# Kernel tuning notes

Hardware: AMD Instinct MI355X
Metric: run time of the kernel (lower is better)

The kernel has to match this reference:

```python
import jax, jax.numpy as jnp
import numpy as np

CODEBOOK_DIM = 12          # log2(codebook_size)
CODEBOOK_SIZE = 4096
DIM = 512
INV_TEMPERATURE = 100.0
CODEBOOK_SCALE = 1.0
DIVERSITY_GAMMA = 1.0
ENTROPY_LOSS_WEIGHT = 0.1
EPS = 1e-5


def setup_inputs() -> dict:
    key = jax.random.key(0)
    k_x, k_wi, k_wo = jax.random.split(key, 3)
    x = jax.random.normal(k_x, (4, 4096, DIM), dtype=jnp.float32)
    # nn.Linear weights: (out_features, in_features)
    w_in = jax.random.normal(k_wi, (CODEBOOK_DIM, DIM), dtype=jnp.float32) * 0.02
    b_in = jnp.zeros((CODEBOOK_DIM,), dtype=jnp.float32)
    w_out = jax.random.normal(k_wo, (DIM, CODEBOOK_DIM), dtype=jnp.float32) * 0.02
    b_out = jnp.zeros((DIM,), dtype=jnp.float32)
    return {"x": x, "w_in": w_in, "b_in": b_in, "w_out": w_out, "b_out": b_out}


def _entropy(prob):
    return (-prob * jnp.log(jnp.clip(prob, EPS))).sum(axis=-1)


def _make_codebook():
    mask = (2 ** jnp.arange(CODEBOOK_DIM - 1, -1, -1)).astype(jnp.int32)  # [d]
    all_codes = jnp.arange(CODEBOOK_SIZE, dtype=jnp.int32)
    bits = ((all_codes[:, None] & mask) != 0).astype(jnp.float32)  # [cs, d]
    codebook = bits * CODEBOOK_SCALE * 2 - CODEBOOK_SCALE  # {-1, +1}
    return mask, codebook


def reference(x, w_in, b_in, w_out, b_out):
    mask, codebook = _make_codebook()

    # project in: [b, n, dim] -> [b, n, d]
    xp = jnp.einsum('bnd,cd->bnc', x, w_in) + b_in  # c == codebook_dim here

    # sign quantization (num_codebooks = 1, so c-dim is implicit)
    quantized = jnp.where(xp > 0, CODEBOOK_SCALE, -CODEBOOK_SCALE).astype(xp.dtype)
    indices = ((quantized > 0).astype(jnp.int32) * mask).sum(axis=-1)  # [b, n]

    # straight-through estimator (training path)
    x_st = xp + jax.lax.stop_gradient(quantized - xp)

    # entropy aux loss over full codebook (frac_per_sample_entropy = 1.0)
    flat = xp.reshape(-1, CODEBOOK_DIM)  # original (pre-quant) input, [bn, d]
    # -distance * inv_temp = 2 * inv_temp * <x, code>
    logits = (2.0 * INV_TEMPERATURE) * (flat @ codebook.T)  # [bn, cs]
    prob = jax.nn.softmax(logits, axis=-1)
    per_sample_entropy = _entropy(prob).mean()
    avg_prob = prob.mean(axis=0)  # [cs]
    codebook_entropy = _entropy(avg_prob)
    entropy_aux_loss = per_sample_entropy - DIVERSITY_GAMMA * codebook_entropy
    aux_loss = entropy_aux_loss * ENTROPY_LOSS_WEIGHT

    # project out: [b, n, d] -> [b, n, dim]
    out = jnp.einsum('bnc,dc->bnd', x_st, w_out) + b_out
    return out, indices, aux_loss
```

## Files before the change

### kernel.cpp

```cpp
#include <hip/hip_runtime.h>
#include <hip/hip_bf16.h>


#define NS    16384
#define NOUT  (NS*512)
#define AUXO  (NOUT+NS)
#define INVT2 200.0f
#define NBLK  512
#define RBLK  64

template <int CTRL>
__device__ inline float dpp_add(float v) {
  int p = __builtin_amdgcn_update_dpp(0, __float_as_int(v), CTRL, 0xF, 0xF, true);
  return v + __int_as_float(p);
}
__device__ inline float rdlane(float v, int lane) {
  return __int_as_float(__builtin_amdgcn_readlane(__float_as_int(v), lane));
}

__global__ __launch_bounds__(512) void k_table(const float* __restrict__ w_out,
                                               const float* __restrict__ b_out,
                                               float* __restrict__ T) {
  __shared__ float s_wt[6144];
  const int t = threadIdx.x;
  #pragma unroll
  for (int k = 0; k < 12; ++k) s_wt[t + k * 512] = w_out[t * 12 + k];
  __syncthreads();

  const int c = blockIdx.x * 16 + (t >> 5);
  float sg[12];
  #pragma unroll
  for (int d = 0; d < 12; ++d) sg[d] = ((c >> (11 - d)) & 1) ? 1.f : -1.f;

  float4* Trow = (float4*)(T + (size_t)c * 512);
  #pragma unroll
  for (int k4 = 0; k4 < 4; ++k4) {
    const int m = (t & 31) + k4 * 32;
    float4 bo = ((const float4*)b_out)[m];
    float4 o = bo;
    #pragma unroll
    for (int d = 0; d < 12; ++d) {
      float4 w4 = ((const float4*)s_wt)[d * 128 + m];
      o.x += sg[d] * w4.x; o.y += sg[d] * w4.y; o.z += sg[d] * w4.z; o.w += sg[d] * w4.w;
    }
    Trow[m] = o;
  }
}

__global__ __launch_bounds__(512, 4) void k_main(
    const float* __restrict__ x,
    const float* __restrict__ w_in,  const float* __restrict__ b_in,
    const float* __restrict__ T,
    float* __restrict__ out, float* __restrict__ idx_out,
    float* __restrict__ P, float* __restrict__ Csum) {

  __shared__ float s_wi[6144];
  __shared__ float s_phi[32][64];
  __shared__ float s_psi[32][64];
  __shared__ float s_h[8];

  const int t = threadIdx.x;

  #pragma unroll
  for (int k = 0; k < 12; ++k) {
    int f  = t + k * 512;
    int kk = f & 3;
    int q  = f >> 2;
    int sub = q & 15, e4 = (q >> 4) & 7, d = q >> 7;
    int e  = sub * 32 + e4 * 4 + kk;
    s_wi[f] = w_in[d * 512 + e];
  }
  __syncthreads();

  const int wave = t >> 6, lane = t & 63;
  const int g = lane >> 4, sub = lane & 15;

  float bin[12];
  #pragma unroll
  for (int d = 0; d < 12; ++d) bin[d] = b_in[d];

  const int i0 = blockIdx.x * 32 + wave * 4 + g;

  const float4* xr0 = (const float4*)(x + (size_t)i0 * 512 + sub * 32);
  float4 xv0[8];
  #pragma unroll
  for (int e4 = 0; e4 < 8; ++e4) xv0[e4] = xr0[e4];

  float p0[12];
  #pragma unroll
  for (int d = 0; d < 12; ++d) p0[d] = 0.f;
  #pragma unroll
  for (int e4 = 0; e4 < 8; ++e4) {
    #pragma unroll
    for (int d = 0; d < 12; ++d) {
      float4 w4 = ((const float4*)s_wi)[d * 128 + e4 * 16 + sub];
      p0[d] += xv0[e4].x * w4.x + xv0[e4].y * w4.y + xv0[e4].z * w4.z + xv0[e4].w * w4.w;
    }
  }
  #pragma unroll
  for (int d = 0; d < 12; ++d) {
    #pragma unroll
    for (int m = 1; m <= 8; m <<= 1) {
      p0[d] += __shfl_xor(p0[d], m, 16);
    }
    p0[d] += bin[d];
  }

  unsigned idx0 = 0u;
  #pragma unroll
  for (int d = 0; d < 12; ++d) {
    idx0 |= (p0[d] > 0.f ? 1u : 0u) << (11 - d);
  }
  if (sub == 0) {
    idx_out[i0] = (float)idx0;
  }

  {
    const float4* Trow = (const float4*)(T + (size_t)idx0 * 512);
    float4* or0 = (float4*)(out + (size_t)i0 * 512);
    #pragma unroll
    for (int e4 = 0; e4 < 8; ++e4) {
      or0[e4 * 16 + sub] = Trow[e4 * 16 + sub];
    }
  }

  float hacc = 0.f;
  #pragma unroll
  for (int s = 0; s < 4; ++s) {
    float xq[12];
    #pragma unroll
    for (int d = 0; d < 12; ++d) xq[d] = rdlane(p0[d], 16 * s);

    float hi = 0.f, lo = 0.f, ah = 0.f, al = 0.f;
    #pragma unroll
    for (int d = 0; d < 6; ++d) {
      int bh = (lane >> (5 - d)) & 1;
      hi += bh ? xq[d]     : -xq[d];
      lo += bh ? xq[6 + d] : -xq[6 + d];
      ah += fabsf(xq[d]);
      al += fabsf(xq[6 + d]);
    }
    float lhi = INVT2 * (hi - ah);
    float llo = INVT2 * (lo - al);
    float ehi = __expf(lhi);
    float elo = __expf(llo);

    float Shi = ehi, Slo = elo;
    Shi = dpp_add<0xB1>(Shi);  Slo = dpp_add<0xB1>(Slo);
    Shi = dpp_add<0x4E>(Shi);  Slo = dpp_add<0x4E>(Slo);
    Shi = dpp_add<0x141>(Shi); Slo = dpp_add<0x141>(Slo);
    Shi = dpp_add<0x140>(Shi); Slo = dpp_add<0x140>(Slo);
    {
      float r0 = rdlane(Shi, 0), r1 = rdlane(Shi, 16), r2 = rdlane(Shi, 32), r3 = rdlane(Shi, 48);
      Shi = (r0 + r1) + (r2 + r3);
      float q0 = rdlane(Slo, 0), q1 = rdlane(Slo, 16), q2 = rdlane(Slo, 32), q3 = rdlane(Slo, 48);
      Slo = (q0 + q1) + (q2 + q3);
    }

    float phi = ehi / Shi;
    float psi = elo / Slo;
    float lnShi = __logf(Shi), lnSlo = __logf(Slo);
    hacc += phi * (lhi - lnShi) + psi * (llo - lnSlo);

    const int ws = wave * 4 + s;
    s_phi[ws][lane] = phi;
    s_psi[ws][lane] = psi;
  }

  #pragma unroll
  for (int m = 1; m <= 32; m <<= 1) hacc += __shfl_xor(hacc, m);
  if (lane == 0) s_h[wave] = hacc;
  __syncthreads();
  if (t == 0) {
    float hs = 0.f;
    for (int w2 = 0; w2 < 8; ++w2) hs += s_h[w2];
    atomicAdd(Csum, hs);
  }

  const int jb = (t >> 5) * 4;
  const int lb = (t & 31) * 2;
  float a00 = 0.f, a01 = 0.f, a10 = 0.f, a11 = 0.f;
  float a20 = 0.f, a21 = 0.f, a30 = 0.f, a31 = 0.f;
  #pragma unroll 4
  for (int s = 0; s < 32; ++s) {
    float4 ph = *(const float4*)&s_phi[s][jb];
    float2 ps = *(const float2*)&s_psi[s][lb];
    a00 += ph.x * ps.x; a01 += ph.x * ps.y;
    a10 += ph.y * ps.x; a11 += ph.y * ps.y;
    a20 += ph.z * ps.x; a21 += ph.z * ps.y;
    a30 += ph.w * ps.x; a31 += ph.w * ps.y;
  }
  float* Pr = P + (size_t)blockIdx.x * 4096;
  *(float2*)&Pr[(jb + 0) * 64 + lb] = make_float2(a00, a01);
  *(float2*)&Pr[(jb + 1) * 64 + lb] = make_float2(a10, a11);
  *(float2*)&Pr[(jb + 2) * 64 + lb] = make_float2(a20, a21);
  *(float2*)&Pr[(jb + 3) * 64 + lb] = make_float2(a30, a31);
}

__global__ __launch_bounds__(256) void k_reduce(const float* __restrict__ P,
                                                float* __restrict__ scal,
                                                float* __restrict__ aux) {
  __shared__ float red[4][64];
  const int t = threadIdx.x;
  const int c = blockIdx.x * 64 + (t & 63);
  const int rg = t >> 6;
  float s = 0.f;
  #pragma unroll 8
  for (int j = 0; j < 128; ++j) s += P[(size_t)(rg * 128 + j) * 4096 + c];
  red[rg][t & 63] = s;
  __syncthreads();
  if (t < 64) {
    float tot = (red[0][t] + red[1][t]) + (red[2][t] + red[3][t]);
    float pb = tot * (1.f / (float)NS);
    float e = pb * __logf(fmaxf(pb, 1e-5f));
    #pragma unroll
    for (int m = 1; m <= 32; m <<= 1) e += __shfl_xor(e, m);
    if (t == 0) {
      atomicAdd(&scal[1], e);
      __threadfence();
      unsigned done = atomicAdd((unsigned*)&scal[2], 1u);
      if (done == RBLK - 1) {
        float E = atomicAdd(&scal[1], 0.f);
        float C = atomicAdd(&scal[0], 0.f);
        float per_sample_entropy = -C * (1.f / (float)NS);
        float codebook_entropy   = -E;
        aux[0] = 0.1f * (per_sample_entropy - codebook_entropy);
      }
    }
  }
}

extern "C" void kernel_launch(void* const* d_in, const int* in_sizes, int n_in,
                              void* d_out, int out_size, void* d_ws, size_t ws_size,
                              hipStream_t stream) {
  const float* x     = (const float*)d_in[0];
  const float* w_in  = (const float*)d_in[1];
  const float* b_in  = (const float*)d_in[2];
  const float* w_out = (const float*)d_in[3];
  const float* b_out = (const float*)d_in[4];
  float* out = (float*)d_out;

  float* T    = (float*)d_ws;
  float* P    = T + (size_t)4096 * 512;
  float* scal = P + (size_t)NBLK * 4096;

  hipMemsetAsync(scal, 0, 3 * sizeof(float), stream);
  k_table<<<256, 512, 0, stream>>>(w_out, b_out, T);
  k_main<<<NBLK, 512, 0, stream>>>(x, w_in, b_in, T,
                                   out, out + NOUT, P, scal);
  k_reduce<<<RBLK, 256, 0, stream>>>(P, scal, out + AUXO);
}
```

Measured before the change: 118.9 us.

## Split main kernel into projection and entropy kernels, compute output directly

Drops the precomputed 4096x512 output lookup table and computes the out-projection inline from sign bits and shared-memory w_out. Splits the fused kernel into a projection kernel, which handles two rows per 16-lane group and writes the 12-dim projections to a workspace buffer, and a separate entropy kernel that reads them and builds larger 64-sample partial outer products. This removes the table build and the gather reads of table rows, and halves the number of partial-product blocks the final reduction has to sum. The cost is an extra kernel launch, a small projection round trip through global memory, and more register pressure in the projection kernel.

```diff
diff --git a/kernel.cpp b/kernel.cpp
--- a/kernel.cpp
+++ b/kernel.cpp
@@ -6,7 +6,8 @@
 #define NOUT  (NS*512)
 #define AUXO  (NOUT+NS)
 #define INVT2 200.0f
-#define NBLK  512
+#define PBLK  256
+#define EBLK  256
 #define RBLK  64
 
 template <int CTRL>
@@ -18,50 +19,18 @@
   return __int_as_float(__builtin_amdgcn_readlane(__float_as_int(v), lane));
 }
 
-__global__ __launch_bounds__(512) void k_table(const float* __restrict__ w_out,
-                                               const float* __restrict__ b_out,
-                                               float* __restrict__ T) {
-  __shared__ float s_wt[6144];
-  const int t = threadIdx.x;
-  #pragma unroll
-  for (int k = 0; k < 12; ++k) s_wt[t + k * 512] = w_out[t * 12 + k];
-  __syncthreads();
-
-  const int c = blockIdx.x * 16 + (t >> 5);
-  float sg[12];
-  #pragma unroll
-  for (int d = 0; d < 12; ++d) sg[d] = ((c >> (11 - d)) & 1) ? 1.f : -1.f;
-
-  float4* Trow = (float4*)(T + (size_t)c * 512);
-  #pragma unroll
-  for (int k4 = 0; k4 < 4; ++k4) {
-    const int m = (t & 31) + k4 * 32;
-    float4 bo = ((const float4*)b_out)[m];
-    float4 o = bo;
-    #pragma unroll
-    for (int d = 0; d < 12; ++d) {
-      float4 w4 = ((const float4*)s_wt)[d * 128 + m];
-      o.x += sg[d] * w4.x; o.y += sg[d] * w4.y; o.z += sg[d] * w4.z; o.w += sg[d] * w4.w;
-    }
-    Trow[m] = o;
-  }
-}
-
-__global__ __launch_bounds__(512, 4) void k_main(
+__global__ __launch_bounds__(512, 2) void k_proj(
     const float* __restrict__ x,
     const float* __restrict__ w_in,  const float* __restrict__ b_in,
-    const float* __restrict__ T,
+    const float* __restrict__ w_out, const float* __restrict__ b_out,
     float* __restrict__ out, float* __restrict__ idx_out,
-    float* __restrict__ P, float* __restrict__ Csum) {
+    float* __restrict__ xp_out) {
 
   __shared__ float s_wi[6144];
-  __shared__ float s_phi[32][64];
-  __shared__ float s_psi[32][64];
-  __shared__ float s_h[8];
+  __shared__ float s_wt[6144];
 
   const int t = threadIdx.x;
 
-  #pragma unroll
   for (int k = 0; k < 12; ++k) {
     int f  = t + k * 512;
     int kk = f & 3;
@@ -69,6 +38,7 @@
     int sub = q & 15, e4 = (q >> 4) & 7, d = q >> 7;
     int e  = sub * 32 + e4 * 4 + kk;
     s_wi[f] = w_in[d * 512 + e];
+    s_wt[f] = w_out[t * 12 + k];
   }
   __syncthreads();
 
@@ -79,22 +49,25 @@
   #pragma unroll
   for (int d = 0; d < 12; ++d) bin[d] = b_in[d];
 
-  const int i0 = blockIdx.x * 32 + wave * 4 + g;
+  const int i0 = blockIdx.x * 64 + wave * 8 + g;
+  const int i1 = i0 + 4;
 
   const float4* xr0 = (const float4*)(x + (size_t)i0 * 512 + sub * 32);
-  float4 xv0[8];
-  #pragma unroll
-  for (int e4 = 0; e4 < 8; ++e4) xv0[e4] = xr0[e4];
-
-  float p0[12];
-  #pragma unroll
-  for (int d = 0; d < 12; ++d) p0[d] = 0.f;
+  const float4* xr1 = (const float4*)(x + (size_t)i1 * 512 + sub * 32);
+  float4 xv0[8], xv1[8];
+  #pragma unroll
+  for (int e4 = 0; e4 < 8; ++e4) { xv0[e4] = xr0[e4]; xv1[e4] = xr1[e4]; }
+
+  float p0[12], p1[12];
+  #pragma unroll
+  for (int d = 0; d < 12; ++d) { p0[d] = 0.f; p1[d] = 0.f; }
   #pragma unroll
   for (int e4 = 0; e4 < 8; ++e4) {
     #pragma unroll
     for (int d = 0; d < 12; ++d) {
       float4 w4 = ((const float4*)s_wi)[d * 128 + e4 * 16 + sub];
       p0[d] += xv0[e4].x * w4.x + xv0[e4].y * w4.y + xv0[e4].z * w4.z + xv0[e4].w * w4.w;
+      p1[d] += xv1[e4].x * w4.x + xv1[e4].y * w4.y + xv1[e4].z * w4.z + xv1[e4].w * w4.w;
     }
   }
   #pragma unroll
@@ -102,34 +75,78 @@
     #pragma unroll
     for (int m = 1; m <= 8; m <<= 1) {
       p0[d] += __shfl_xor(p0[d], m, 16);
+      p1[d] += __shfl_xor(p1[d], m, 16);
     }
     p0[d] += bin[d];
-  }
-
-  unsigned idx0 = 0u;
+    p1[d] += bin[d];
+  }
+
+  unsigned idx0 = 0u, idx1 = 0u;
   #pragma unroll
   for (int d = 0; d < 12; ++d) {
     idx0 |= (p0[d] > 0.f ? 1u : 0u) << (11 - d);
+    idx1 |= (p1[d] > 0.f ? 1u : 0u) << (11 - d);
   }
   if (sub == 0) {
     idx_out[i0] = (float)idx0;
+    idx_out[i1] = (float)idx1;
   }
 
   {
-    const float4* Trow = (const float4*)(T + (size_t)idx0 * 512);
-    float4* or0 = (float4*)(out + (size_t)i0 * 512);
-    #pragma unroll
-    for (int e4 = 0; e4 < 8; ++e4) {
-      or0[e4 * 16 + sub] = Trow[e4 * 16 + sub];
-    }
-  }
+    float4 v0 = make_float4(p0[0], p0[1], p0[2], p0[3]);
+    float4 v1 = make_float4(p1[0], p1[1], p1[2], p1[3]);
+    if (sub == 1) { v0 = make_float4(p0[4], p0[5], p0[6], p0[7]);
+                    v1 = make_float4(p1[4], p1[5], p1[6], p1[7]); }
+    if (sub == 2) { v0 = make_float4(p0[8], p0[9], p0[10], p0[11]);
+                    v1 = make_float4(p1[8], p1[9], p1[10], p1[11]); }
+    if (sub < 3) {
+      ((float4*)(xp_out + (size_t)i0 * 12))[sub] = v0;
+      ((float4*)(xp_out + (size_t)i1 * 12))[sub] = v1;
+    }
+  }
+
+  float sg0[12], sg1[12];
+  #pragma unroll
+  for (int d = 0; d < 12; ++d) {
+    sg0[d] = p0[d] > 0.f ? 1.f : -1.f;
+    sg1[d] = p1[d] > 0.f ? 1.f : -1.f;
+  }
+  float4* or0 = (float4*)(out + (size_t)i0 * 512);
+  float4* or1 = (float4*)(out + (size_t)i1 * 512);
+  #pragma unroll
+  for (int e4 = 0; e4 < 8; ++e4) {
+    float4 bo = ((const float4*)b_out)[e4 * 16 + sub];
+    float4 o0 = bo, o1 = bo;
+    #pragma unroll
+    for (int d = 0; d < 12; ++d) {
+      float4 w4 = ((const float4*)s_wt)[d * 128 + e4 * 16 + sub];
+      o0.x += sg0[d] * w4.x; o0.y += sg0[d] * w4.y; o0.z += sg0[d] * w4.z; o0.w += sg0[d] * w4.w;
+      o1.x += sg1[d] * w4.x; o1.y += sg1[d] * w4.y; o1.z += sg1[d] * w4.z; o1.w += sg1[d] * w4.w;
+    }
+    or0[e4 * 16 + sub] = o0;
+    or1[e4 * 16 + sub] = o1;
+  }
+}
+
+__global__ __launch_bounds__(512) void k_ent(
+    const float* __restrict__ xp,
+    float* __restrict__ P, float* __restrict__ scal) {
+
+  __shared__ float s_phi[64][64];
+  __shared__ float s_psi[64][64];
+  __shared__ float s_h[8];
+
+  const int t = threadIdx.x;
+  const int wave = t >> 6, lane = t & 63;
+  const int sbase = blockIdx.x * 64 + wave * 8;
 
   float hacc = 0.f;
-  #pragma unroll
-  for (int s = 0; s < 4; ++s) {
+  #pragma unroll 1
+  for (int s = 0; s < 8; ++s) {
+    const float* xps = xp + (size_t)(sbase + s) * 12;
     float xq[12];
     #pragma unroll
-    for (int d = 0; d < 12; ++d) xq[d] = rdlane(p0[d], 16 * s);
+    for (int d = 0; d < 12; ++d) xq[d] = xps[d];
 
     float hi = 0.f, lo = 0.f, ah = 0.f, al = 0.f;
     #pragma unroll
@@ -162,9 +179,8 @@
     float lnShi = __logf(Shi), lnSlo = __logf(Slo);
     hacc += phi * (lhi - lnShi) + psi * (llo - lnSlo);
 
-    const int ws = wave * 4 + s;
-    s_phi[ws][lane] = phi;
-    s_psi[ws][lane] = psi;
+    s_phi[wave * 8 + s][lane] = phi;
+    s_psi[wave * 8 + s][lane] = psi;
   }
 
   #pragma unroll
@@ -174,7 +190,7 @@
   if (t == 0) {
     float hs = 0.f;
     for (int w2 = 0; w2 < 8; ++w2) hs += s_h[w2];
-    atomicAdd(Csum, hs);
+    atomicAdd(&scal[0], hs);
   }
 
   const int jb = (t >> 5) * 4;
@@ -182,7 +198,7 @@
   float a00 = 0.f, a01 = 0.f, a10 = 0.f, a11 = 0.f;
   float a20 = 0.f, a21 = 0.f, a30 = 0.f, a31 = 0.f;
   #pragma unroll 4
-  for (int s = 0; s < 32; ++s) {
+  for (int s = 0; s < 64; ++s) {
     float4 ph = *(const float4*)&s_phi[s][jb];
     float2 ps = *(const float2*)&s_psi[s][lb];
     a00 += ph.x * ps.x; a01 += ph.x * ps.y;
@@ -206,7 +222,7 @@
   const int rg = t >> 6;
   float s = 0.f;
   #pragma unroll 8
-  for (int j = 0; j < 128; ++j) s += P[(size_t)(rg * 128 + j) * 4096 + c];
+  for (int j = 0; j < 64; ++j) s += P[(size_t)(rg * 64 + j) * 4096 + c];
   red[rg][t & 63] = s;
   __syncthreads();
   if (t < 64) {
@@ -240,13 +256,13 @@
   const float* b_out = (const float*)d_in[4];
   float* out = (float*)d_out;
 
-  float* T    = (float*)d_ws;
-  float* P    = T + (size_t)4096 * 512;
-  float* scal = P + (size_t)NBLK * 4096;
+  float* P    = (float*)d_ws;
+  float* xp   = P + (size_t)EBLK * 4096;
+  float* scal = xp + (size_t)NS * 12;
 
   hipMemsetAsync(scal, 0, 3 * sizeof(float), stream);
-  k_table<<<256, 512, 0, stream>>>(w_out, b_out, T);
-  k_main<<<NBLK, 512, 0, stream>>>(x, w_in, b_in, T,
-                                   out, out + NOUT, P, scal);
+  k_proj<<<PBLK, 512, 0, stream>>>(x, w_in, b_in, w_out, b_out,
+                                   out, out + NOUT, xp);
+  k_ent<<<EBLK, 512, 0, stream>>>(xp, P, scal);
   k_reduce<<<RBLK, 256, 0, stream>>>(P, scal, out + AUXO);
 }
```

Measured after the change: 116.1 us. 2.4% less time.

## Restructure into fused table+projection kernel and entropy+gather kernel, drop memset

Applied to the files above, without the earlier changes.

Folds the codebook-output table build into the same launch as the input projection, using block ranges so both run concurrently, and clears the scalar accumulators in-kernel instead of with a memset. The projected 12-dim values go to a workspace buffer. A second kernel then splits blocks between the entropy/outer-product work (64 samples per block, fewer partial rows) and the gather of output rows from the table. This removes the serial dependency of the main kernel on the table build and cuts the partial-reduction size, at the cost of an extra global round-trip for the projections and indices.

```diff
diff --git a/kernel.cpp b/kernel.cpp
--- a/kernel.cpp
+++ b/kernel.cpp
@@ -6,7 +6,10 @@
 #define NOUT  (NS*512)
 #define AUXO  (NOUT+NS)
 #define INVT2 200.0f
-#define NBLK  512
+#define TBLK  64
+#define DBLK  1024
+#define EBLK  256
+#define GBLK  512
 #define RBLK  64
 
 template <int CTRL>
@@ -18,57 +21,54 @@
   return __int_as_float(__builtin_amdgcn_readlane(__float_as_int(v), lane));
 }
 
-__global__ __launch_bounds__(512) void k_table(const float* __restrict__ w_out,
-                                               const float* __restrict__ b_out,
-                                               float* __restrict__ T) {
-  __shared__ float s_wt[6144];
-  const int t = threadIdx.x;
-  #pragma unroll
-  for (int k = 0; k < 12; ++k) s_wt[t + k * 512] = w_out[t * 12 + k];
-  __syncthreads();
-
-  const int c = blockIdx.x * 16 + (t >> 5);
-  float sg[12];
-  #pragma unroll
-  for (int d = 0; d < 12; ++d) sg[d] = ((c >> (11 - d)) & 1) ? 1.f : -1.f;
-
-  float4* Trow = (float4*)(T + (size_t)c * 512);
-  #pragma unroll
-  for (int k4 = 0; k4 < 4; ++k4) {
-    const int m = (t & 31) + k4 * 32;
-    float4 bo = ((const float4*)b_out)[m];
-    float4 o = bo;
-    #pragma unroll
-    for (int d = 0; d < 12; ++d) {
-      float4 w4 = ((const float4*)s_wt)[d * 128 + m];
-      o.x += sg[d] * w4.x; o.y += sg[d] * w4.y; o.z += sg[d] * w4.z; o.w += sg[d] * w4.w;
-    }
-    Trow[m] = o;
-  }
-}
-
-__global__ __launch_bounds__(512, 4) void k_main(
+__global__ __launch_bounds__(256) void kA(
     const float* __restrict__ x,
     const float* __restrict__ w_in,  const float* __restrict__ b_in,
-    const float* __restrict__ T,
-    float* __restrict__ out, float* __restrict__ idx_out,
-    float* __restrict__ P, float* __restrict__ Csum) {
-
-  __shared__ float s_wi[6144];
-  __shared__ float s_phi[32][64];
-  __shared__ float s_psi[32][64];
-  __shared__ float s_h[8];
-
-  const int t = threadIdx.x;
-
-  #pragma unroll
-  for (int k = 0; k < 12; ++k) {
-    int f  = t + k * 512;
-    int kk = f & 3;
-    int q  = f >> 2;
-    int sub = q & 15, e4 = (q >> 4) & 7, d = q >> 7;
-    int e  = sub * 32 + e4 * 4 + kk;
-    s_wi[f] = w_in[d * 512 + e];
+    const float* __restrict__ w_out, const float* __restrict__ b_out,
+    float* __restrict__ T, float* __restrict__ idx_out,
+    float* __restrict__ xp_out, float* __restrict__ scal) {
+
+  __shared__ float s_w[6144];
+  const int bid = blockIdx.x;
+  const int t   = threadIdx.x;
+
+  if (bid < TBLK) {
+    #pragma unroll
+    for (int k = 0; k < 12; ++k) {
+      s_w[t + k * 512]         = w_out[t * 12 + k];
+      s_w[t + 256 + k * 512]   = w_out[(t + 256) * 12 + k];
+    }
+    if (bid == 0 && t == 0) { scal[0] = 0.f; scal[1] = 0.f; ((unsigned*)scal)[2] = 0u; }
+    __syncthreads();
+
+    const int c = bid * 64 + (t >> 2);
+    float sg[12];
+    #pragma unroll
+    for (int d = 0; d < 12; ++d) sg[d] = ((c >> (11 - d)) & 1) ? 1.f : -1.f;
+
+    float4* Trow = (float4*)(T + (size_t)c * 512);
+    const float4* bo4 = (const float4*)b_out;
+    const float4* wt4 = (const float4*)s_w;
+    #pragma unroll 8
+    for (int j = 0; j < 32; ++j) {
+      const int m = (t & 3) + 4 * j;
+      float4 o = bo4[m];
+      #pragma unroll
+      for (int d = 0; d < 12; ++d) {
+        float4 w4 = wt4[d * 128 + m];
+        o.x += sg[d] * w4.x; o.y += sg[d] * w4.y; o.z += sg[d] * w4.z; o.w += sg[d] * w4.w;
+      }
+      Trow[m] = o;
+    }
+    return;
+  }
+
+  #pragma unroll
+  for (int k = 0; k < 24; ++k) {
+    const int f = t + k * 256;
+    const int d = f >> 9, e = f & 511;
+    const int pos = ((d * 128 + ((e >> 2) & 7) * 16 + (e >> 5)) << 2) | (e & 3);
+    s_w[pos] = w_in[f];
   }
   __syncthreads();
 
@@ -79,7 +79,7 @@
   #pragma unroll
   for (int d = 0; d < 12; ++d) bin[d] = b_in[d];
 
-  const int i0 = blockIdx.x * 32 + wave * 4 + g;
+  const int i0 = (bid - TBLK) * 16 + wave * 4 + g;
 
   const float4* xr0 = (const float4*)(x + (size_t)i0 * 512 + sub * 32);
   float4 xv0[8];
@@ -93,43 +93,64 @@
   for (int e4 = 0; e4 < 8; ++e4) {
     #pragma unroll
     for (int d = 0; d < 12; ++d) {
-      float4 w4 = ((const float4*)s_wi)[d * 128 + e4 * 16 + sub];
+      float4 w4 = ((const float4*)s_w)[d * 128 + e4 * 16 + sub];
       p0[d] += xv0[e4].x * w4.x + xv0[e4].y * w4.y + xv0[e4].z * w4.z + xv0[e4].w * w4.w;
     }
   }
   #pragma unroll
   for (int d = 0; d < 12; ++d) {
     #pragma unroll
-    for (int m = 1; m <= 8; m <<= 1) {
-      p0[d] += __shfl_xor(p0[d], m, 16);
-    }
+    for (int m = 1; m <= 8; m <<= 1) p0[d] += __shfl_xor(p0[d], m, 16);
     p0[d] += bin[d];
   }
 
   unsigned idx0 = 0u;
   #pragma unroll
-  for (int d = 0; d < 12; ++d) {
-    idx0 |= (p0[d] > 0.f ? 1u : 0u) << (11 - d);
-  }
-  if (sub == 0) {
-    idx_out[i0] = (float)idx0;
-  }
+  for (int d = 0; d < 12; ++d) idx0 |= (p0[d] > 0.f ? 1u : 0u) << (11 - d);
+  if (sub == 0) idx_out[i0] = (float)idx0;
 
   {
-    const float4* Trow = (const float4*)(T + (size_t)idx0 * 512);
-    float4* or0 = (float4*)(out + (size_t)i0 * 512);
-    #pragma unroll
-    for (int e4 = 0; e4 < 8; ++e4) {
-      or0[e4 * 16 + sub] = Trow[e4 * 16 + sub];
-    }
-  }
-
+    float4 v0 = make_float4(p0[0], p0[1], p0[2], p0[3]);
+    if (sub == 1) v0 = make_float4(p0[4], p0[5], p0[6], p0[7]);
+    if (sub == 2) v0 = make_float4(p0[8], p0[9], p0[10], p0[11]);
+    if (sub < 3) ((float4*)(xp_out + (size_t)i0 * 12))[sub] = v0;
+  }
+}
+
+__global__ __launch_bounds__(256) void kB(
+    const float* __restrict__ T, const float* __restrict__ idx_f,
+    const float* __restrict__ xp,
+    float* __restrict__ out, float* __restrict__ P, float* __restrict__ scal) {
+
+  __shared__ float s_phi[64][64];
+  __shared__ float s_psi[64][64];
+  __shared__ float s_h[4];
+
+  const int bid = blockIdx.x, t = threadIdx.x;
+  const int wave = t >> 6, lane = t & 63;
+
+  if (bid >= EBLK) {
+    const int base = (bid - EBLK) * 32 + wave * 8;
+    #pragma unroll
+    for (int r = 0; r < 8; ++r) {
+      const int i = base + r;
+      const unsigned c = (unsigned)idx_f[i];
+      const float4* Tr = (const float4*)(T + (size_t)c * 512);
+      float4* orow = (float4*)(out + (size_t)i * 512);
+      orow[lane]      = Tr[lane];
+      orow[lane + 64] = Tr[lane + 64];
+    }
+    return;
+  }
+
+  const int sbase = bid * 64 + wave * 16;
   float hacc = 0.f;
-  #pragma unroll
-  for (int s = 0; s < 4; ++s) {
+  #pragma unroll 1
+  for (int s = 0; s < 16; ++s) {
+    const float* xps = xp + (size_t)(sbase + s) * 12;
     float xq[12];
     #pragma unroll
-    for (int d = 0; d < 12; ++d) xq[d] = rdlane(p0[d], 16 * s);
+    for (int d = 0; d < 12; ++d) xq[d] = xps[d];
 
     float hi = 0.f, lo = 0.f, ah = 0.f, al = 0.f;
     #pragma unroll
@@ -162,51 +183,45 @@
     float lnShi = __logf(Shi), lnSlo = __logf(Slo);
     hacc += phi * (lhi - lnShi) + psi * (llo - lnSlo);
 
-    const int ws = wave * 4 + s;
-    s_phi[ws][lane] = phi;
-    s_psi[ws][lane] = psi;
+    s_phi[wave * 16 + s][lane] = phi;
+    s_psi[wave * 16 + s][lane] = psi;
   }
 
   #pragma unroll
   for (int m = 1; m <= 32; m <<= 1) hacc += __shfl_xor(hacc, m);
   if (lane == 0) s_h[wave] = hacc;
   __syncthreads();
-  if (t == 0) {
-    float hs = 0.f;
-    for (int w2 = 0; w2 < 8; ++w2) hs += s_h[w2];
-    atomicAdd(Csum, hs);
-  }
-
-  const int jb = (t >> 5) * 4;
-  const int lb = (t & 31) * 2;
-  float a00 = 0.f, a01 = 0.f, a10 = 0.f, a11 = 0.f;
-  float a20 = 0.f, a21 = 0.f, a30 = 0.f, a31 = 0.f;
+  if (t == 0) atomicAdd(&scal[0], (s_h[0] + s_h[1]) + (s_h[2] + s_h[3]));
+
+  const int jb = (t >> 4) * 4;
+  const int lb = (t & 15) * 4;
+  float4 r0 = {0,0,0,0}, r1 = {0,0,0,0}, r2 = {0,0,0,0}, r3 = {0,0,0,0};
   #pragma unroll 4
-  for (int s = 0; s < 32; ++s) {
+  for (int s = 0; s < 64; ++s) {
     float4 ph = *(const float4*)&s_phi[s][jb];
-    float2 ps = *(const float2*)&s_psi[s][lb];
-    a00 += ph.x * ps.x; a01 += ph.x * ps.y;
-    a10 += ph.y * ps.x; a11 += ph.y * ps.y;
-    a20 += ph.z * ps.x; a21 += ph.z * ps.y;
-    a30 += ph.w * ps.x; a31 += ph.w * ps.y;
-  }
-  float* Pr = P + (size_t)blockIdx.x * 4096;
-  *(float2*)&Pr[(jb + 0) * 64 + lb] = make_float2(a00, a01);
-  *(float2*)&Pr[(jb + 1) * 64 + lb] = make_float2(a10, a11);
-  *(float2*)&Pr[(jb + 2) * 64 + lb] = make_float2(a20, a21);
-  *(float2*)&Pr[(jb + 3) * 64 + lb] = make_float2(a30, a31);
-}
-
-__global__ __launch_bounds__(256) void k_reduce(const float* __restrict__ P,
-                                                float* __restrict__ scal,
-                                                float* __restrict__ aux) {
+    float4 ps = *(const float4*)&s_psi[s][lb];
+    r0.x += ph.x * ps.x; r0.y += ph.x * ps.y; r0.z += ph.x * ps.z; r0.w += ph.x * ps.w;
+    r1.x += ph.y * ps.x; r1.y += ph.y * ps.y; r1.z += ph.y * ps.z; r1.w += ph.y * ps.w;
+    r2.x += ph.z * ps.x; r2.y += ph.z * ps.y; r2.z += ph.z * ps.z; r2.w += ph.z * ps.w;
+    r3.x += ph.w * ps.x; r3.y += ph.w * ps.y; r3.z += ph.w * ps.z; r3.w += ph.w * ps.w;
+  }
+  float* Pr = P + (size_t)bid * 4096;
+  *(float4*)&Pr[(jb + 0) * 64 + lb] = r0;
+  *(float4*)&Pr[(jb + 1) * 64 + lb] = r1;
+  *(float4*)&Pr[(jb + 2) * 64 + lb] = r2;
+  *(float4*)&Pr[(jb + 3) * 64 + lb] = r3;
+}
+
+__global__ __launch_bounds__(256) void kC(const float* __restrict__ P,
+                                          float* __restrict__ scal,
+                                          float* __restrict__ aux) {
   __shared__ float red[4][64];
   const int t = threadIdx.x;
   const int c = blockIdx.x * 64 + (t & 63);
   const int rg = t >> 6;
   float s = 0.f;
   #pragma unroll 8
-  for (int j = 0; j < 128; ++j) s += P[(size_t)(rg * 128 + j) * 4096 + c];
+  for (int j = 0; j < 64; ++j) s += P[(size_t)(rg * 64 + j) * 4096 + c];
   red[rg][t & 63] = s;
   __syncthreads();
   if (t < 64) {
@@ -238,15 +253,16 @@
   const float* b_in  = (const float*)d_in[2];
   const float* w_out = (const float*)d_in[3];
   const float* b_out = (const float*)d_in[4];
-  float* out = (float*)d_out;
+  float* out     = (float*)d_out;
+  float* idx_out = out + NOUT;
+  float* aux     = out + AUXO;
 
   float* T    = (float*)d_ws;
   float* P    = T + (size_t)4096 * 512;
-  float* scal = P + (size_t)NBLK * 4096;
-
-  hipMemsetAsync(scal, 0, 3 * sizeof(float), stream);
-  k_table<<<256, 512, 0, stream>>>(w_out, b_out, T);
-  k_main<<<NBLK, 512, 0, stream>>>(x, w_in, b_in, T,
-                                   out, out + NOUT, P, scal);
-  k_reduce<<<RBLK, 256, 0, stream>>>(P, scal, out + AUXO);
-}
+  float* xp   = P + (size_t)EBLK * 4096;
+  float* scal = xp + (size_t)NS * 12;
+
+  kA<<<TBLK + DBLK, 256, 0, stream>>>(x, w_in, b_in, w_out, b_out, T, idx_out, xp, scal);
+  kB<<<EBLK + GBLK, 256, 0, stream>>>(T, idx_out, xp, out, P, scal);
+  kC<<<RBLK, 256, 0, stream>>>(P, scal, aux);
+}
```

Result: slower. 122.6 us (+3.1%).
